# Kernel tuning notes

Measured on AMD Instinct MI355X. Metric: run time of the kernel, lower is better.

## Reference

```python
import jax, jax.numpy as jnp
import numpy as np


def setup_inputs() -> dict:
    key = jax.random.key(0)
    k1, k2 = jax.random.split(key)
    pred = jax.random.normal(k1, (8, 4096, 3), dtype=jnp.float32)
    target = jax.random.normal(k2, (8, 4096, 3), dtype=jnp.float32)
    return {"pred": pred, "target": target}


def reference(pred, target):
    # Squared L2 pairwise distances without materializing (B,N,M,3) diff:
    # ||p - t||^2 = ||p||^2 + ||t||^2 - 2 p.t
    p2 = jnp.sum(pred ** 2, axis=-1)            # (B, N)
    t2 = jnp.sum(target ** 2, axis=-1)          # (B, M)
    cross = jnp.einsum('bnd,bmd->bnm', pred, target)  # (B, N, M)
    dist = p2[:, :, None] + t2[:, None, :] - 2.0 * cross  # (B, N, M)
    min_pred_to_target = jnp.min(dist, axis=2)  # (B, N)
    min_target_to_pred = jnp.min(dist, axis=1)  # (B, M)
    return jnp.mean(min_pred_to_target) + jnp.mean(min_target_to_pred)
```

## Files before the change

kernel.cpp:

```cpp
#include <hip/hip_runtime.h>


#define BATCH 8
#define NPTS  4096
#define TPB   512
#define QPT   8
#define NQG   16
#define QB    (NQG * QPT)
#define NSL   32
#define NBLK  (2 * BATCH * (NPTS / QB))
#define PHPTS 2048
#define SLICE (PHPTS / NSL)

#define INNER_LOOP(SBASE)                                                     \
    _Pragma("unroll 4")                                                       \
    for (int i = 0; i < SLICE; i += 2) {                                      \
        float4 t0 = (SBASE)[i];                                               \
        float4 t1 = (SBASE)[i + 1];                                           \
        _Pragma("unroll")                                                     \
        for (int k = 0; k < QPT; ++k) {                                       \
            float d0 = fmaf(az[k], t0.z, fmaf(ay[k], t0.y, fmaf(ax[k], t0.x, t0.w))); \
            float d1 = fmaf(az[k], t1.z, fmaf(ay[k], t1.y, fmaf(ax[k], t1.x, t1.w))); \
            mn[k] = fminf(fminf(d0, d1), mn[k]);                              \
        }                                                                     \
    }

__global__ __launch_bounds__(TPB, 4)
void chamfer_main(const float* __restrict__ pred,
                  const float* __restrict__ tgt,
                  float* __restrict__ blkpart )
{
    int bid = blockIdx.x;
    int dir = bid >> 8;
    int b   = (bid >> 5) & 7;
    int qt  = bid & 31;

    const float* qsrc = dir ? tgt  : pred;
    const float* csrc = dir ? pred : tgt;

    __shared__ float4 sc[PHPTS];
    __shared__ float  acc[TPB / 64];

    int tid = threadIdx.x;
    int qg  = tid & (NQG - 1);
    int sl  = tid >> 4;

    const float4* q4 = reinterpret_cast<const float4*>(
        qsrc + ((size_t)b * NPTS + (size_t)qt * QB) * 3);
    float4 v0 = q4[qg * 6 + 0];
    float4 v1 = q4[qg * 6 + 1];
    float4 v2 = q4[qg * 6 + 2];
    float4 v3 = q4[qg * 6 + 3];
    float4 v4 = q4[qg * 6 + 4];
    float4 v5 = q4[qg * 6 + 5];

    float ax[QPT], ay[QPT], az[QPT], mn[QPT];
    {
        float qx[QPT], qy[QPT], qz[QPT];
        qx[0]=v0.x; qy[0]=v0.y; qz[0]=v0.z;
        qx[1]=v0.w; qy[1]=v1.x; qz[1]=v1.y;
        qx[2]=v1.z; qy[2]=v1.w; qz[2]=v2.x;
        qx[3]=v2.y; qy[3]=v2.z; qz[3]=v2.w;
        qx[4]=v3.x; qy[4]=v3.y; qz[4]=v3.z;
        qx[5]=v3.w; qy[5]=v4.x; qz[5]=v4.y;
        qx[6]=v4.z; qy[6]=v4.w; qz[6]=v5.x;
        qx[7]=v5.y; qy[7]=v5.z; qz[7]=v5.w;
#pragma unroll
        for (int i = 0; i < QPT; ++i) {
            ax[i] = -2.0f * qx[i];
            ay[i] = -2.0f * qy[i];
            az[i] = -2.0f * qz[i];
            mn[i] = 3.0e38f;
        }
    }

    const float4* t4 = reinterpret_cast<const float4*>(csrc + (size_t)b * NPTS * 3);

    float4 r0 = t4[tid * 3 + 0];
    float4 r1 = t4[tid * 3 + 1];
    float4 r2 = t4[tid * 3 + 2];
    sc[tid*4+0] = make_float4(r0.x, r0.y, r0.z, r0.x*r0.x + r0.y*r0.y + r0.z*r0.z);
    sc[tid*4+1] = make_float4(r0.w, r1.x, r1.y, r0.w*r0.w + r1.x*r1.x + r1.y*r1.y);
    sc[tid*4+2] = make_float4(r1.z, r1.w, r2.x, r1.z*r1.z + r1.w*r1.w + r2.x*r2.x);
    sc[tid*4+3] = make_float4(r2.y, r2.z, r2.w, r2.y*r2.y + r2.z*r2.z + r2.w*r2.w);
    __syncthreads();

    float4 s0 = t4[1536 + tid * 3 + 0];
    float4 s1 = t4[1536 + tid * 3 + 1];
    float4 s2 = t4[1536 + tid * 3 + 2];

    {
        const float4* sbase = sc + sl * SLICE;
        INNER_LOOP(sbase)
    }
    __syncthreads();

    sc[tid*4+0] = make_float4(s0.x, s0.y, s0.z, s0.x*s0.x + s0.y*s0.y + s0.z*s0.z);
    sc[tid*4+1] = make_float4(s0.w, s1.x, s1.y, s0.w*s0.w + s1.x*s1.x + s1.y*s1.y);
    sc[tid*4+2] = make_float4(s1.z, s1.w, s2.x, s1.z*s1.z + s1.w*s1.w + s2.x*s2.x);
    sc[tid*4+3] = make_float4(s2.y, s2.z, s2.w, s2.y*s2.y + s2.z*s2.z + s2.w*s2.w);
    __syncthreads();

    {
        const float4* sbase = sc + sl * SLICE;
        INNER_LOOP(sbase)
    }
    __syncthreads();

    float* scratch = (float*)sc;
#pragma unroll
    for (int r = 0; r < QPT; ++r)
        scratch[sl * QB + qg * QPT + r] = mn[r];
    __syncthreads();

    float val = 0.0f;
    if (tid < QB) {
        float m = scratch[tid];
#pragma unroll 8
        for (int s = 1; s < NSL; ++s)
            m = fminf(m, scratch[s * QB + tid]);
        const float* qp = qsrc + ((size_t)b * NPTS + (size_t)qt * QB + tid) * 3;
        float x = qp[0], y = qp[1], z = qp[2];
        val = x*x + y*y + z*z + m;
    }
#pragma unroll
    for (int o = 32; o; o >>= 1) val += __shfl_down(val, o);
    int lane = tid & 63, wid = tid >> 6;
    if (lane == 0) acc[wid] = val;
    __syncthreads();
    if (tid == 0) {
        float s = 0.0f;
#pragma unroll
        for (int i = 0; i < TPB / 64; ++i) s += acc[i];
        blkpart[bid] = s;
    }
}

__global__ __launch_bounds__(TPB)
void chamfer_final(const float* __restrict__ blkpart,
                   float* __restrict__ out)
{
    float s = blkpart[threadIdx.x];
#pragma unroll
    for (int o = 32; o; o >>= 1) s += __shfl_down(s, o);
    __shared__ float acc[TPB / 64];
    int lane = threadIdx.x & 63, wid = threadIdx.x >> 6;
    if (lane == 0) acc[wid] = s;
    __syncthreads();
    if (threadIdx.x == 0) {
        float t = 0.0f;
#pragma unroll
        for (int i = 0; i < TPB / 64; ++i) t += acc[i];
        out[0] = t * (1.0f / (BATCH * NPTS));
    }
}

#define FTPB  256
#define CHUNK 512
#define NCH   (NPTS / CHUNK)

__global__ __launch_bounds__(FTPB)
void chamfer_fallback(const float* __restrict__ pred,
                      const float* __restrict__ tgt,
                      float* __restrict__ out)
{
    int bid = blockIdx.x;
    const int per_dir = BATCH * (NPTS / FTPB);
    int dir = bid / per_dir;
    int r   = bid - dir * per_dir;
    int b   = r / (NPTS / FTPB);
    int qt  = r % (NPTS / FTPB);

    const float* qsrc = dir ? tgt  : pred;
    const float* csrc = dir ? pred : tgt;

    __shared__ float4 sc[CHUNK];
    int q = qt * FTPB + threadIdx.x;
    const float* qp = qsrc + (size_t)(b * NPTS + q) * 3;
    float x = qp[0], y = qp[1], z = qp[2];
    float ax = -2.0f * x, ay = -2.0f * y, az = -2.0f * z;
    float w = x * x + y * y + z * z;
    float mn = 3.0e38f;

    for (int ch = 0; ch < NCH; ++ch) {
        __syncthreads();
        const float* cbase = csrc + (size_t)(b * NPTS + ch * CHUNK) * 3;
        for (int p = threadIdx.x; p < CHUNK; p += FTPB) {
            float tx = cbase[3 * p + 0];
            float ty = cbase[3 * p + 1];
            float tz = cbase[3 * p + 2];
            sc[p] = make_float4(tx, ty, tz, tx * tx + ty * ty + tz * tz);
        }
        __syncthreads();
#pragma unroll 4
        for (int j = 0; j < CHUNK; ++j) {
            float4 t = sc[j];
            float d = fmaf(az, t.z, fmaf(ay, t.y, fmaf(ax, t.x, t.w)));
            mn = fminf(mn, d);
        }
    }
    mn += w;
#pragma unroll
    for (int o = 32; o; o >>= 1) mn += __shfl_down(mn, o);
    __shared__ float acc[FTPB / 64];
    int lane = threadIdx.x & 63, wid = threadIdx.x >> 6;
    if (lane == 0) acc[wid] = mn;
    __syncthreads();
    if (threadIdx.x == 0) {
        float s = 0.0f;
#pragma unroll
        for (int i = 0; i < FTPB / 64; ++i) s += acc[i];
        atomicAdd(out, s * (1.0f / (BATCH * NPTS)));
    }
}

extern "C" void kernel_launch(void* const* d_in, const int* in_sizes, int n_in,
                              void* d_out, int out_size, void* d_ws, size_t ws_size,
                              hipStream_t stream)
{
    const float* pred = (const float*)d_in[0];
    const float* tgt  = (const float*)d_in[1];
    float* out = (float*)d_out;

    if (ws_size >= NBLK * sizeof(float)) {
        float* blkpart = (float*)d_ws;
        chamfer_main<<<NBLK, TPB, 0, stream>>>(pred, tgt, blkpart);
        chamfer_final<<<1, TPB, 0, stream>>>(blkpart, out);
    } else {
        hipMemsetAsync(d_out, 0, sizeof(float), stream);
        chamfer_fallback<<<2 * BATCH * (NPTS / FTPB), FTPB, 0, stream>>>(pred, tgt, out);
    }
}
```

Before: 28.80 us.

## Use packed float2 FMA with 16 queries per thread and staggered LDS slices

```diff
diff --git a/kernel.cpp b/kernel.cpp
--- a/kernel.cpp
+++ b/kernel.cpp
@@ -1,27 +1,41 @@
 #include <hip/hip_runtime.h>
 
+
+typedef float v2f __attribute__((ext_vector_type(2)));
 
 #define BATCH 8
 #define NPTS  4096
 #define TPB   512
-#define QPT   8
-#define NQG   16
+#define QPT   16
+#define NQG   8
 #define QB    (NQG * QPT)
-#define NSL   32
+#define NSL   64
 #define NBLK  (2 * BATCH * (NPTS / QB))
 #define PHPTS 2048
 #define SLICE (PHPTS / NSL)
-
-#define INNER_LOOP(SBASE)                                                     \
+#define SPAIR (SLICE / 2)
+#define RSTR  (QB + 1)
+
+#define INNER_LOOP(BASE)                                                      \
     _Pragma("unroll 4")                                                       \
-    for (int i = 0; i < SLICE; i += 2) {                                      \
-        float4 t0 = (SBASE)[i];                                               \
-        float4 t1 = (SBASE)[i + 1];                                           \
+    for (int jj = 0; jj < SPAIR; ++jj) {                                      \
+        int idx = ((jj + sl) & (SPAIR - 1)) * 2;                              \
+        float4 t0 = (BASE)[idx];                                              \
+        float4 t1 = (BASE)[idx + 1];                                          \
+        v2f xx0 = {t0.x, t0.x}, yy0 = {t0.y, t0.y};                           \
+        v2f zz0 = {t0.z, t0.z}, ww0 = {t0.w, t0.w};                           \
+        v2f xx1 = {t1.x, t1.x}, yy1 = {t1.y, t1.y};                           \
+        v2f zz1 = {t1.z, t1.z}, ww1 = {t1.w, t1.w};                           \
         _Pragma("unroll")                                                     \
-        for (int k = 0; k < QPT; ++k) {                                       \
-            float d0 = fmaf(az[k], t0.z, fmaf(ay[k], t0.y, fmaf(ax[k], t0.x, t0.w))); \
-            float d1 = fmaf(az[k], t1.z, fmaf(ay[k], t1.y, fmaf(ax[k], t1.x, t1.w))); \
-            mn[k] = fminf(fminf(d0, d1), mn[k]);                              \
+        for (int i = 0; i < 8; ++i) {                                         \
+            v2f da = __builtin_elementwise_fma(azp[i], zz0, ww0);             \
+            da = __builtin_elementwise_fma(ayp[i], yy0, da);                  \
+            da = __builtin_elementwise_fma(axp[i], xx0, da);                  \
+            v2f db = __builtin_elementwise_fma(azp[i], zz1, ww1);             \
+            db = __builtin_elementwise_fma(ayp[i], yy1, db);                  \
+            db = __builtin_elementwise_fma(axp[i], xx1, db);                  \
+            mn[2*i]   = fminf(fminf(da.x, db.x), mn[2*i]);        \
+            mn[2*i+1] = fminf(fminf(da.y, db.y), mn[2*i+1]);      \
         }                                                                     \
     }
 
@@ -38,39 +52,32 @@
     const float* qsrc = dir ? tgt  : pred;
     const float* csrc = dir ? pred : tgt;
 
-    __shared__ float4 sc[PHPTS];
-    __shared__ float  acc[TPB / 64];
+    __shared__ __align__(16) float lds_raw[NSL * RSTR];
+    __shared__ float acc[TPB / 64];
+    float4* sc = (float4*)lds_raw;
+    float*  scratch = lds_raw;
 
     int tid = threadIdx.x;
     int qg  = tid & (NQG - 1);
-    int sl  = tid >> 4;
+    int sl  = tid >> 3;
 
     const float4* q4 = reinterpret_cast<const float4*>(
         qsrc + ((size_t)b * NPTS + (size_t)qt * QB) * 3);
-    float4 v0 = q4[qg * 6 + 0];
-    float4 v1 = q4[qg * 6 + 1];
-    float4 v2 = q4[qg * 6 + 2];
-    float4 v3 = q4[qg * 6 + 3];
-    float4 v4 = q4[qg * 6 + 4];
-    float4 v5 = q4[qg * 6 + 5];
-
-    float ax[QPT], ay[QPT], az[QPT], mn[QPT];
+    v2f axp[8], ayp[8], azp[8];
+    float mn[QPT];
     {
-        float qx[QPT], qy[QPT], qz[QPT];
-        qx[0]=v0.x; qy[0]=v0.y; qz[0]=v0.z;
-        qx[1]=v0.w; qy[1]=v1.x; qz[1]=v1.y;
-        qx[2]=v1.z; qy[2]=v1.w; qz[2]=v2.x;
-        qx[3]=v2.y; qy[3]=v2.z; qz[3]=v2.w;
-        qx[4]=v3.x; qy[4]=v3.y; qz[4]=v3.z;
-        qx[5]=v3.w; qy[5]=v4.x; qz[5]=v4.y;
-        qx[6]=v4.z; qy[6]=v4.w; qz[6]=v5.x;
-        qx[7]=v5.y; qy[7]=v5.z; qz[7]=v5.w;
-#pragma unroll
-        for (int i = 0; i < QPT; ++i) {
-            ax[i] = -2.0f * qx[i];
-            ay[i] = -2.0f * qy[i];
-            az[i] = -2.0f * qz[i];
-            mn[i] = 3.0e38f;
+        float f[48];
+#pragma unroll
+        for (int k = 0; k < 12; ++k) {
+            float4 u = q4[qg * 12 + k];
+            f[4*k+0] = u.x; f[4*k+1] = u.y; f[4*k+2] = u.z; f[4*k+3] = u.w;
+        }
+#pragma unroll
+        for (int i = 0; i < 8; ++i) {
+            axp[i] = (v2f){-2.0f * f[6*i+0], -2.0f * f[6*i+3]};
+            ayp[i] = (v2f){-2.0f * f[6*i+1], -2.0f * f[6*i+4]};
+            azp[i] = (v2f){-2.0f * f[6*i+2], -2.0f * f[6*i+5]};
+            mn[2*i] = 3.0e38f; mn[2*i+1] = 3.0e38f;
         }
     }
 
@@ -90,8 +97,8 @@
     float4 s2 = t4[1536 + tid * 3 + 2];
 
     {
-        const float4* sbase = sc + sl * SLICE;
-        INNER_LOOP(sbase)
+        const float4* base = sc + sl * SLICE;
+        INNER_LOOP(base)
     }
     __syncthreads();
 
@@ -102,15 +109,14 @@
     __syncthreads();
 
     {
-        const float4* sbase = sc + sl * SLICE;
-        INNER_LOOP(sbase)
-    }
-    __syncthreads();
-
-    float* scratch = (float*)sc;
+        const float4* base = sc + sl * SLICE;
+        INNER_LOOP(base)
+    }
+    __syncthreads();
+
 #pragma unroll
     for (int r = 0; r < QPT; ++r)
-        scratch[sl * QB + qg * QPT + r] = mn[r];
+        scratch[sl * RSTR + qg * QPT + r] = mn[r];
     __syncthreads();
 
     float val = 0.0f;
@@ -118,7 +124,7 @@
         float m = scratch[tid];
 #pragma unroll 8
         for (int s = 1; s < NSL; ++s)
-            m = fminf(m, scratch[s * QB + tid]);
+            m = fminf(m, scratch[s * RSTR + tid]);
         const float* qp = qsrc + ((size_t)b * NPTS + (size_t)qt * QB + tid) * 3;
         float x = qp[0], y = qp[1], z = qp[2];
         val = x*x + y*y + z*z + m;
```

Result: slower. 32.57 us (+13.1%).
